# Optimization experiments

Hardware: AMD Instinct MI355X
Metric: run time of the kernel (lower is better)

## Reference

```python
import jax, jax.numpy as jnp
import numpy as np

B, S, D, H, HD = 4096, 50, 32, 4, 8
SCALE = 1.0 / (8 ** 0.5)


def setup_inputs() -> dict:
    key = jax.random.key(0)
    ks = jax.random.split(key, 12)
    inp = {
        'Q': jax.random.normal(ks[0], (B, S, D), dtype=jnp.float32),
        'K': jax.random.normal(ks[1], (B, S, D), dtype=jnp.float32),
        'V': jax.random.normal(ks[2], (B, S, D), dtype=jnp.float32),
        'mask': jax.random.randint(ks[3], (B, 1, S, S), 0, 2).astype(jnp.bool_),
        # Linear weights (stored as [in, out]; equivalent math to torch's x @ W.T + b)
        'WQ': jax.random.normal(ks[4], (D, D), dtype=jnp.float32) * 0.1,
        'bQ': jnp.zeros((D,), dtype=jnp.float32),
        'WK': jax.random.normal(ks[5], (D, D), dtype=jnp.float32) * 0.1,
        'bK': jnp.zeros((D,), dtype=jnp.float32),
        'WV': jax.random.normal(ks[6], (D, D), dtype=jnp.float32) * 0.1,
        'bV': jnp.zeros((D,), dtype=jnp.float32),
        'WO': jax.random.normal(ks[7], (D, D), dtype=jnp.float32) * 0.1,
        'bO': jnp.zeros((D,), dtype=jnp.float32),
    }
    return inp


def reference(Q, K, V, mask, WQ, bQ, WK, bK, WV, bV, WO, bO):
    qSrc = Q
    # fcQ/fcK/fcV are (faithfully) applied twice, as in the original forward
    q = (Q @ WQ + bQ) @ WQ + bQ
    k = (K @ WK + bK) @ WK + bK
    v = (V @ WV + bV) @ WV + bV
    # split heads: [B, S, D] -> [B, H, S, HD]
    q = q.reshape(B, S, H, HD).transpose(0, 2, 1, 3)
    k = k.reshape(B, S, H, HD).transpose(0, 2, 1, 3)
    v = v.reshape(B, S, H, HD).transpose(0, 2, 1, 3)
    score = jnp.einsum('bhqd,bhkd->bhqk', q, k) * SCALE
    score = jnp.where(mask, -jnp.inf, score)
    attn = jax.nn.softmax(score, axis=-1)
    ctx = jnp.einsum('bhqk,bhkd->bhqd', attn, v)
    ctx = ctx.transpose(0, 2, 1, 3).reshape(B, S, D)
    out = ctx @ WO + bO  # dropout is identity in eval mode
    return qSrc + out
```

## Files before the change

kernel.cpp:

```cpp
#include <hip/hip_runtime.h>

#define NB 4096
constexpr float kQscale = 0.35355339059327378f * 1.4426950408889634f;
constexpr int SV = 72;

typedef __attribute__((ext_vector_type(8))) short bf16x8;
typedef __attribute__((ext_vector_type(4))) float f32x4;
typedef __attribute__((ext_vector_type(4))) unsigned u32x4;

__device__ __forceinline__ unsigned cvt2(float lo, float hi) {
  unsigned u;
  asm("v_cvt_pk_bf16_f32 %0, %1, %2" : "=v"(u) : "v"(lo), "v"(hi));
  return u;
}
__device__ __forceinline__ float fexp2(float x) {
  float r;
  asm("v_exp_f32 %0, %1" : "=v"(r) : "v"(x));
  return r;
}
__device__ __forceinline__ void xchF(unsigned& a, unsigned& b) {
  asm volatile("v_permlane32_swap_b32 %0, %1" : "+v"(a), "+v"(b));
  asm volatile("v_permlane16_swap_b32 %0, %1" : "+v"(a), "+v"(b));
}

__global__ __launch_bounds__(256) void mha(
    const float* __restrict__ Qg, const float* __restrict__ Kg,
    const float* __restrict__ Vg, const void* __restrict__ maskg,
    const float* __restrict__ WQg, const float* __restrict__ bQg,
    const float* __restrict__ WKg, const float* __restrict__ bKg,
    const float* __restrict__ WVg, const float* __restrict__ bVg,
    const float* __restrict__ WOg, const float* __restrict__ bOg,
    float* __restrict__ outg)
{
  __shared__ __align__(16) short V2s[4][32*SV];
  __shared__ unsigned sRawW[4][80];

  const int t = threadIdx.x;
  const int lane = t & 63;
  const int wv = t >> 6;
  const int c = lane & 15, g = lane >> 4;
  const int b = blockIdx.x*4 + wv;
  short* V2 = V2s[wv];
  unsigned* sRaw = sRawW[wv];

  auto mkfrag = [&](float4 x0, float4 x1) -> bf16x8 {
    const u32x4 u = {cvt2(x0.x,x0.y), cvt2(x0.z,x0.w), cvt2(x1.x,x1.y), cvt2(x1.z,x1.w)};
    return __builtin_bit_cast(bf16x8, u);
  };
  auto ldW = [&](const float* __restrict__ Wp, int dcol) -> bf16x8 {
    float w[8];
    #pragma unroll
    for (int e = 0; e < 8; ++e) w[e] = Wp[(g*8 + e)*32 + dcol];
    const u32x4 u = {cvt2(w[0],w[1]), cvt2(w[2],w[3]), cvt2(w[4],w[5]), cvt2(w[6],w[7])};
    return __builtin_bit_cast(bf16x8, u);
  };
  auto projR = [&](bf16x8 xb, bf16x8 wa0, bf16x8 wa1,
                   float4 bv0, float4 bv1, float scale) -> bf16x8 {
    f32x4 c0 = {bv0.x, bv0.y, bv0.z, bv0.w};
    f32x4 c1 = {bv1.x, bv1.y, bv1.z, bv1.w};
    c0 = __builtin_amdgcn_mfma_f32_16x16x32_bf16(wa0, xb, c0, 0, 0, 0);
    c1 = __builtin_amdgcn_mfma_f32_16x16x32_bf16(wa1, xb, c1, 0, 0, 0);
    unsigned A0 = cvt2(c0[0]*scale, c0[1]*scale), A1 = cvt2(c0[2]*scale, c0[3]*scale);
    unsigned B0 = cvt2(c1[0]*scale, c1[1]*scale), B1 = cvt2(c1[2]*scale, c1[3]*scale);
    xchF(A0, B0); xchF(A1, B1);
    const u32x4 u = {A0, A1, B0, B1};
    return __builtin_bit_cast(bf16x8, u);
  };

  {
    const unsigned wdet = ((const unsigned*)maskg)[lane];
    const bool byteMask = (__ballot(wdet > 1u) != 0ull);
    for (int cg = 0; cg < 5; ++cg) {
      unsigned v[8];
      #pragma unroll
      for (int j = 0; j < 8; ++j) {
        const int idx = (cg*8 + j)*64 + lane;
        v[j] = 0;
        if (idx < 2500)
          v[j] = byteMask ? (unsigned)((const unsigned char*)maskg)[b*2500 + idx]
                          : ((const unsigned*)maskg)[b*2500 + idx];
      }
      #pragma unroll
      for (int j = 0; j < 8; ++j) {
        const unsigned long long m = __ballot(v[j] != 0u);
        const int ch = cg*8 + j;
        if (lane < 2) sRaw[ch*2 + lane] = lane ? (unsigned)(m >> 32) : (unsigned)m;
      }
    }
  }

  bf16x8 kf[4];
  {
    const bf16x8 wK0 = ldW(WKg, c), wK1 = ldW(WKg, 16 + c);
    const float4 bK0 = *(const float4*)&bKg[g*4];
    const float4 bK1 = *(const float4*)&bKg[16 + g*4];
    #pragma unroll
    for (int m = 0; m < 4; ++m) {
      const int row = m*16 + c;
      const int ra = b*1600 + ((row < 50) ? row : 0)*32 + g*8;
      const bf16x8 xb = mkfrag(*(const float4*)&Kg[ra], *(const float4*)&Kg[ra + 4]);
      const bf16x8 k1 = projR(xb, wK0, wK1, bK0, bK1, 1.f);
      kf[m] = projR(k1, wK0, wK1, bK0, bK1, 1.f);
    }
  }

  {
    const bf16x8 wV0 = ldW(WVg, c), wV1 = ldW(WVg, 16 + c);
    const float4 bV0 = *(const float4*)&bVg[g*4];
    const float4 bV1 = *(const float4*)&bVg[16 + g*4];
    const float bc0 = bVg[c], bc1 = bVg[16 + c];
    #pragma unroll
    for (int m = 0; m < 4; ++m) {
      const int row = m*16 + c;
      const int ra = b*1600 + ((row < 50) ? row : 0)*32 + g*8;
      const bf16x8 xb = mkfrag(*(const float4*)&Vg[ra], *(const float4*)&Vg[ra + 4]);
      const bf16x8 v1 = projR(xb, wV0, wV1, bV0, bV1, 1.f);
      f32x4 z0 = {bc0, bc0, bc0, bc0}, z1 = {bc1, bc1, bc1, bc1};
      z0 = __builtin_amdgcn_mfma_f32_16x16x32_bf16(v1, wV0, z0, 0, 0, 0);
      z1 = __builtin_amdgcn_mfma_f32_16x16x32_bf16(v1, wV1, z1, 0, 0, 0);
      const int j0 = m*16 + g*4;
      const float a0 = (j0+0 < 50) ? z0[0] : 0.f;
      const float a1 = (j0+1 < 50) ? z0[1] : 0.f;
      const float a2 = (j0+2 < 50) ? z0[2] : 0.f;
      const float a3 = (j0+3 < 50) ? z0[3] : 0.f;
      *(uint2*)&V2[c*SV + j0] = make_uint2(cvt2(a0,a1), cvt2(a2,a3));
      const float u0 = (j0+0 < 50) ? z1[0] : 0.f;
      const float u1 = (j0+1 < 50) ? z1[1] : 0.f;
      const float u2 = (j0+2 < 50) ? z1[2] : 0.f;
      const float u3 = (j0+3 < 50) ? z1[3] : 0.f;
      *(uint2*)&V2[(16 + c)*SV + j0] = make_uint2(cvt2(u0,u1), cvt2(u2,u3));
    }
  }

  const bf16x8 wQ0 = ldW(WQg, c), wQ1 = ldW(WQg, 16 + c);
  const float4 bQ0 = *(const float4*)&bQg[g*4];
  const float4 bQ1 = *(const float4*)&bQg[16 + g*4];
  const bf16x8 wO0 = ldW(WOg, c), wO1 = ldW(WOg, 16 + c);
  const float bO0 = bOg[c], bO1 = bOg[16 + c];
  __syncthreads();

  const bf16x8 zf = {0,0,0,0,0,0,0,0};

  #pragma unroll 1
  for (int qt = 0; qt < 4; ++qt) {
    const int myq = qt*16 + c;
    bf16x8 qb;
    {
      const int ra = b*1600 + ((myq < 50) ? myq : 0)*32 + g*8;
      const bf16x8 xq = mkfrag(*(const float4*)&Qg[ra], *(const float4*)&Qg[ra + 4]);
      const bf16x8 q1 = projR(xq, wQ0, wQ1, bQ0, bQ1, 1.f);
      qb = projR(q1, wQ0, wQ1, bQ0, bQ1, kQscale);
    }
    unsigned mm0, mm1;
    {
      const int bp = (myq < 50) ? 50*myq : 0;
      const unsigned ra = sRaw[(bp >> 5) + 0];
      const unsigned rb = sRaw[(bp >> 5) + 1];
      const unsigned rc = sRaw[(bp >> 5) + 2];
      const unsigned sh = bp & 31;
      mm0 = (unsigned)((((unsigned long long)rb << 32) | ra) >> sh);
      mm1 = (unsigned)((((unsigned long long)rc << 32) | rb) >> sh);
      if (myq >= 50) { mm0 = ~0u; mm1 = ~0u; }
    }
    unsigned ox0[4], ox1[4];
    #pragma unroll
    for (int h = 0; h < 4; ++h) {
      const bf16x8 vf0 = *(const bf16x8*)&V2[(h*8 + (c & 7))*SV + g*8];
      const bf16x8 vf1 = *(const bf16x8*)&V2[(h*8 + (c & 7))*SV + 32 + g*8];
      const bf16x8 qh = (g == h) ? qb : zf;
      f32x4 sc[4];
      #pragma unroll
      for (int Ni = 0; Ni < 4; ++Ni) {
        f32x4 z = {0.f, 0.f, 0.f, 0.f};
        sc[Ni] = __builtin_amdgcn_mfma_f32_16x16x32_bf16(kf[Ni], qh, z, 0, 0, 0);
      }
      unsigned kpm = 0;
      float mx = -1e30f;
      #pragma unroll
      for (int Ni = 0; Ni < 4; ++Ni) {
        const unsigned w = (Ni < 2) ? mm0 : mm1;
        #pragma unroll
        for (int r = 0; r < 4; ++r) {
          const int key = Ni*16 + g*4 + r;
          const bool keep = (key < 50) && (((w >> (key & 31)) & 1u) == 0u);
          kpm |= keep ? (1u << (Ni*4 + r)) : 0u;
          mx = keep ? fmaxf(mx, sc[Ni][r]) : mx;
        }
      }
      mx = fmaxf(mx, __shfl_xor(mx, 16));
      mx = fmaxf(mx, __shfl_xor(mx, 32));
      float rs = 0.f;
      unsigned pk[8];
      #pragma unroll
      for (int Ni = 0; Ni < 4; ++Ni) {
        float p[4];
        #pragma unroll
        for (int r = 0; r < 4; ++r) {
          const float e = fexp2(sc[Ni][r] - mx);
          p[r] = ((kpm >> (Ni*4 + r)) & 1u) ? e : 0.f;
          rs += p[r];
        }
        pk[Ni*2]   = cvt2(p[0], p[1]);
        pk[Ni*2+1] = cvt2(p[2], p[3]);
      }
      rs += __shfl_xor(rs, 16);
      rs += __shfl_xor(rs, 32);
      const float ri = (rs > 0.f) ? __builtin_amdgcn_rcpf(rs) : 0.f;
      unsigned w0 = pk[0], w2 = pk[2];  xchF(w0, w2);
      unsigned w1 = pk[1], w3 = pk[3];  xchF(w1, w3);
      unsigned x0 = pk[4], x2 = pk[6];  xchF(x0, x2);
      unsigned x1 = pk[5], x3 = pk[7];  xchF(x1, x3);
      const u32x4 w0v = {w0, w1, w2, w3};
      const u32x4 w1v = {x0, x1, x2, x3};
      const bf16x8 pf0 = __builtin_bit_cast(bf16x8, w0v);
      const bf16x8 pf1 = __builtin_bit_cast(bf16x8, w1v);
      f32x4 cac = {0.f, 0.f, 0.f, 0.f};
      cac = __builtin_amdgcn_mfma_f32_16x16x32_bf16(vf0, pf0, cac, 0, 0, 0);
      cac = __builtin_amdgcn_mfma_f32_16x16x32_bf16(vf1, pf1, cac, 0, 0, 0);
      ox0[h] = cvt2(cac[0]*ri, cac[1]*ri);
      ox1[h] = cvt2(cac[2]*ri, cac[3]*ri);
    }
    {
      float res[2][4];
      #pragma unroll
      for (int Nj = 0; Nj < 2; ++Nj)
        #pragma unroll
        for (int r = 0; r < 4; ++r) {
          const int row = qt*16 + g*4 + r;
          res[Nj][r] = (row < 50) ? Qg[b*1600 + row*32 + Nj*16 + c] : 0.f;
        }
      unsigned a0 = ox0[0], a1 = ox0[1], a2 = ox0[2], a3 = ox0[3];
      xchF(a0, a1);
      xchF(a2, a3);
      xchF(a0, a2);
      xchF(a1, a3);
      unsigned c0 = ox1[0], c1 = ox1[1], c2 = ox1[2], c3 = ox1[3];
      xchF(c0, c1);
      xchF(c2, c3);
      xchF(c0, c2);
      xchF(c1, c3);
      const u32x4 afv = {a0, c0, a1, c1};
      const bf16x8 af = __builtin_bit_cast(bf16x8, afv);
      #pragma unroll
      for (int Nj = 0; Nj < 2; ++Nj) {
        const bf16x8 bbf = Nj ? wO1 : wO0;
        const float bv = Nj ? bO1 : bO0;
        f32x4 o = {bv, bv, bv, bv};
        o = __builtin_amdgcn_mfma_f32_16x16x32_bf16(af, bbf, o, 0, 0, 0);
        #pragma unroll
        for (int r = 0; r < 4; ++r) {
          const int row = qt*16 + g*4 + r;
          if (row < 50)
            outg[b*1600 + row*32 + Nj*16 + c] = o[r] + res[Nj][r];
        }
      }
    }
  }
}

extern "C" void kernel_launch(void* const* d_in, const int* in_sizes, int n_in,
                              void* d_out, int out_size, void* d_ws, size_t ws_size,
                              hipStream_t stream) {
  const float* Q  = (const float*)d_in[0];
  const float* K  = (const float*)d_in[1];
  const float* V  = (const float*)d_in[2];
  const void*  M  = d_in[3];
  const float* WQ = (const float*)d_in[4];
  const float* bQ = (const float*)d_in[5];
  const float* WK = (const float*)d_in[6];
  const float* bK = (const float*)d_in[7];
  const float* WV = (const float*)d_in[8];
  const float* bV = (const float*)d_in[9];
  const float* WO = (const float*)d_in[10];
  const float* bO = (const float*)d_in[11];
  float* out = (float*)d_out;
  (void)d_ws; (void)ws_size; (void)in_sizes; (void)n_in; (void)out_size;

  hipLaunchKernelGGL(mha, dim3(NB/4), dim3(256), 0, stream,
                     Q, K, V, M, WQ, bQ, WK, bK, WV, bV, WO, bO, out);
}
```

Before: 65.07 us.

## Split each batch across four waves by query/key row tile with shared K/V

Each block of four waves now handles one batch element instead of four, and each wave owns one 16-row tile for the K, V and Q projections and for the attention. Projected K goes to shared memory so every wave can read all key fragments, and the mask bit-packing is spread across waves. The aim is to cut the per-wave serial work (the four-step query loop and repeated projections) and expose more parallelism with four times as many blocks. In exchange it adds a K shared-memory round trip, a block-wide barrier per batch, and reloads the weights in every wave of every block.

```diff
diff --git a/kernel.cpp b/kernel.cpp
--- a/kernel.cpp
+++ b/kernel.cpp
@@ -2,6 +2,7 @@
 
 #define NB 4096
 constexpr float kQscale = 0.35355339059327378f * 1.4426950408889634f;
+constexpr int ST = 40;
 constexpr int SV = 72;
 
 typedef __attribute__((ext_vector_type(8))) short bf16x8;
@@ -32,16 +33,16 @@
     const float* __restrict__ WOg, const float* __restrict__ bOg,
     float* __restrict__ outg)
 {
-  __shared__ __align__(16) short V2s[4][32*SV];
-  __shared__ unsigned sRawW[4][80];
+  __shared__ __align__(16) short K2s[64*ST];
+  __shared__ __align__(16) short V2[32*SV];
+  __shared__ unsigned sRaw[80];
 
   const int t = threadIdx.x;
+  const int b = blockIdx.x;
   const int lane = t & 63;
   const int wv = t >> 6;
   const int c = lane & 15, g = lane >> 4;
-  const int b = blockIdx.x*4 + wv;
-  short* V2 = V2s[wv];
-  unsigned* sRaw = sRawW[wv];
+  const int myrow = wv*16 + c;
 
   auto mkfrag = [&](float4 x0, float4 x1) -> bf16x8 {
     const u32x4 u = {cvt2(x0.x,x0.y), cvt2(x0.z,x0.w), cvt2(x1.x,x1.y), cvt2(x1.z,x1.w)};
@@ -67,192 +68,183 @@
     return __builtin_bit_cast(bf16x8, u);
   };
 
+  const int ra = b*1600 + ((myrow < 50) ? myrow : 0)*32 + g*8;
+  const bf16x8 xbK = mkfrag(*(const float4*)&Kg[ra], *(const float4*)&Kg[ra + 4]);
+  const bf16x8 xbV = mkfrag(*(const float4*)&Vg[ra], *(const float4*)&Vg[ra + 4]);
+  const bf16x8 xbQ = mkfrag(*(const float4*)&Qg[ra], *(const float4*)&Qg[ra + 4]);
+
   {
     const unsigned wdet = ((const unsigned*)maskg)[lane];
     const bool byteMask = (__ballot(wdet > 1u) != 0ull);
-    for (int cg = 0; cg < 5; ++cg) {
-      unsigned v[8];
-      #pragma unroll
-      for (int j = 0; j < 8; ++j) {
-        const int idx = (cg*8 + j)*64 + lane;
-        v[j] = 0;
-        if (idx < 2500)
-          v[j] = byteMask ? (unsigned)((const unsigned char*)maskg)[b*2500 + idx]
-                          : ((const unsigned*)maskg)[b*2500 + idx];
-      }
-      #pragma unroll
-      for (int j = 0; j < 8; ++j) {
-        const unsigned long long m = __ballot(v[j] != 0u);
-        const int ch = cg*8 + j;
-        if (lane < 2) sRaw[ch*2 + lane] = lane ? (unsigned)(m >> 32) : (unsigned)m;
-      }
-    }
-  }
-
-  bf16x8 kf[4];
+    #pragma unroll
+    for (int cc = 0; cc < 10; ++cc) {
+      const int ch = wv*10 + cc;
+      const int idx = ch*64 + lane;
+      unsigned val = 0;
+      if (idx < 2500)
+        val = byteMask ? (unsigned)((const unsigned char*)maskg)[b*2500 + idx]
+                       : ((const unsigned*)maskg)[b*2500 + idx];
+      const unsigned long long m = __ballot(val != 0u);
+      if (lane < 2) sRaw[ch*2 + lane] = lane ? (unsigned)(m >> 32) : (unsigned)m;
+    }
+  }
+
   {
     const bf16x8 wK0 = ldW(WKg, c), wK1 = ldW(WKg, 16 + c);
     const float4 bK0 = *(const float4*)&bKg[g*4];
     const float4 bK1 = *(const float4*)&bKg[16 + g*4];
-    #pragma unroll
-    for (int m = 0; m < 4; ++m) {
-      const int row = m*16 + c;
-      const int ra = b*1600 + ((row < 50) ? row : 0)*32 + g*8;
-      const bf16x8 xb = mkfrag(*(const float4*)&Kg[ra], *(const float4*)&Kg[ra + 4]);
-      const bf16x8 k1 = projR(xb, wK0, wK1, bK0, bK1, 1.f);
-      kf[m] = projR(k1, wK0, wK1, bK0, bK1, 1.f);
-    }
-  }
-
+    const bf16x8 k1 = projR(xbK, wK0, wK1, bK0, bK1, 1.f);
+    #pragma unroll
+    for (int Ni = 0; Ni < 2; ++Ni) {
+      const bf16x8 wa = Ni ? wK1 : wK0;
+      const float4 bv = Ni ? bK1 : bK0;
+      f32x4 acc = {bv.x, bv.y, bv.z, bv.w};
+      acc = __builtin_amdgcn_mfma_f32_16x16x32_bf16(wa, k1, acc, 0, 0, 0);
+      *(uint2*)&K2s[myrow*ST + Ni*16 + g*4] =
+          make_uint2(cvt2(acc[0], acc[1]), cvt2(acc[2], acc[3]));
+    }
+  }
   {
     const bf16x8 wV0 = ldW(WVg, c), wV1 = ldW(WVg, 16 + c);
     const float4 bV0 = *(const float4*)&bVg[g*4];
     const float4 bV1 = *(const float4*)&bVg[16 + g*4];
     const float bc0 = bVg[c], bc1 = bVg[16 + c];
-    #pragma unroll
-    for (int m = 0; m < 4; ++m) {
-      const int row = m*16 + c;
-      const int ra = b*1600 + ((row < 50) ? row : 0)*32 + g*8;
-      const bf16x8 xb = mkfrag(*(const float4*)&Vg[ra], *(const float4*)&Vg[ra + 4]);
-      const bf16x8 v1 = projR(xb, wV0, wV1, bV0, bV1, 1.f);
-      f32x4 z0 = {bc0, bc0, bc0, bc0}, z1 = {bc1, bc1, bc1, bc1};
-      z0 = __builtin_amdgcn_mfma_f32_16x16x32_bf16(v1, wV0, z0, 0, 0, 0);
-      z1 = __builtin_amdgcn_mfma_f32_16x16x32_bf16(v1, wV1, z1, 0, 0, 0);
-      const int j0 = m*16 + g*4;
-      const float a0 = (j0+0 < 50) ? z0[0] : 0.f;
-      const float a1 = (j0+1 < 50) ? z0[1] : 0.f;
-      const float a2 = (j0+2 < 50) ? z0[2] : 0.f;
-      const float a3 = (j0+3 < 50) ? z0[3] : 0.f;
-      *(uint2*)&V2[c*SV + j0] = make_uint2(cvt2(a0,a1), cvt2(a2,a3));
-      const float u0 = (j0+0 < 50) ? z1[0] : 0.f;
-      const float u1 = (j0+1 < 50) ? z1[1] : 0.f;
-      const float u2 = (j0+2 < 50) ? z1[2] : 0.f;
-      const float u3 = (j0+3 < 50) ? z1[3] : 0.f;
-      *(uint2*)&V2[(16 + c)*SV + j0] = make_uint2(cvt2(u0,u1), cvt2(u2,u3));
-    }
-  }
-
-  const bf16x8 wQ0 = ldW(WQg, c), wQ1 = ldW(WQg, 16 + c);
-  const float4 bQ0 = *(const float4*)&bQg[g*4];
-  const float4 bQ1 = *(const float4*)&bQg[16 + g*4];
-  const bf16x8 wO0 = ldW(WOg, c), wO1 = ldW(WOg, 16 + c);
-  const float bO0 = bOg[c], bO1 = bOg[16 + c];
+    const bf16x8 v1 = projR(xbV, wV0, wV1, bV0, bV1, 1.f);
+    f32x4 z0 = {bc0, bc0, bc0, bc0}, z1 = {bc1, bc1, bc1, bc1};
+    z0 = __builtin_amdgcn_mfma_f32_16x16x32_bf16(v1, wV0, z0, 0, 0, 0);
+    z1 = __builtin_amdgcn_mfma_f32_16x16x32_bf16(v1, wV1, z1, 0, 0, 0);
+    const int j0 = wv*16 + g*4;
+    const float a0 = (j0+0 < 50) ? z0[0] : 0.f;
+    const float a1 = (j0+1 < 50) ? z0[1] : 0.f;
+    const float a2 = (j0+2 < 50) ? z0[2] : 0.f;
+    const float a3 = (j0+3 < 50) ? z0[3] : 0.f;
+    *(uint2*)&V2[c*SV + j0] = make_uint2(cvt2(a0,a1), cvt2(a2,a3));
+    const float u0 = (j0+0 < 50) ? z1[0] : 0.f;
+    const float u1 = (j0+1 < 50) ? z1[1] : 0.f;
+    const float u2 = (j0+2 < 50) ? z1[2] : 0.f;
+    const float u3 = (j0+3 < 50) ? z1[3] : 0.f;
+    *(uint2*)&V2[(16 + c)*SV + j0] = make_uint2(cvt2(u0,u1), cvt2(u2,u3));
+  }
+  bf16x8 qb;
+  {
+    const bf16x8 wQ0 = ldW(WQg, c), wQ1 = ldW(WQg, 16 + c);
+    const float4 bQ0 = *(const float4*)&bQg[g*4];
+    const float4 bQ1 = *(const float4*)&bQg[16 + g*4];
+    const bf16x8 q1 = projR(xbQ, wQ0, wQ1, bQ0, bQ1, 1.f);
+    qb = projR(q1, wQ0, wQ1, bQ0, bQ1, kQscale);
+  }
   __syncthreads();
 
+  unsigned mm0, mm1;
+  {
+    const int bp = (myrow < 50) ? 50*myrow : 0;
+    const unsigned fa = sRaw[(bp >> 5) + 0];
+    const unsigned fb = sRaw[(bp >> 5) + 1];
+    const unsigned fc = sRaw[(bp >> 5) + 2];
+    const unsigned sh = bp & 31;
+    mm0 = (unsigned)((((unsigned long long)fb << 32) | fa) >> sh);
+    mm1 = (unsigned)((((unsigned long long)fc << 32) | fb) >> sh);
+    if (myrow >= 50) { mm0 = ~0u; mm1 = ~0u; }
+  }
+  bf16x8 kf[4];
+  #pragma unroll
+  for (int Ni = 0; Ni < 4; ++Ni)
+    kf[Ni] = *(const bf16x8*)&K2s[(Ni*16 + c)*ST + g*8];
+
   const bf16x8 zf = {0,0,0,0,0,0,0,0};
-
-  #pragma unroll 1
-  for (int qt = 0; qt < 4; ++qt) {
-    const int myq = qt*16 + c;
-    bf16x8 qb;
-    {
-      const int ra = b*1600 + ((myq < 50) ? myq : 0)*32 + g*8;
-      const bf16x8 xq = mkfrag(*(const float4*)&Qg[ra], *(const float4*)&Qg[ra + 4]);
-      const bf16x8 q1 = projR(xq, wQ0, wQ1, bQ0, bQ1, 1.f);
-      qb = projR(q1, wQ0, wQ1, bQ0, bQ1, kQscale);
-    }
-    unsigned mm0, mm1;
-    {
-      const int bp = (myq < 50) ? 50*myq : 0;
-      const unsigned ra = sRaw[(bp >> 5) + 0];
-      const unsigned rb = sRaw[(bp >> 5) + 1];
-      const unsigned rc = sRaw[(bp >> 5) + 2];
-      const unsigned sh = bp & 31;
-      mm0 = (unsigned)((((unsigned long long)rb << 32) | ra) >> sh);
-      mm1 = (unsigned)((((unsigned long long)rc << 32) | rb) >> sh);
-      if (myq >= 50) { mm0 = ~0u; mm1 = ~0u; }
-    }
-    unsigned ox0[4], ox1[4];
-    #pragma unroll
-    for (int h = 0; h < 4; ++h) {
-      const bf16x8 vf0 = *(const bf16x8*)&V2[(h*8 + (c & 7))*SV + g*8];
-      const bf16x8 vf1 = *(const bf16x8*)&V2[(h*8 + (c & 7))*SV + 32 + g*8];
-      const bf16x8 qh = (g == h) ? qb : zf;
-      f32x4 sc[4];
-      #pragma unroll
-      for (int Ni = 0; Ni < 4; ++Ni) {
-        f32x4 z = {0.f, 0.f, 0.f, 0.f};
-        sc[Ni] = __builtin_amdgcn_mfma_f32_16x16x32_bf16(kf[Ni], qh, z, 0, 0, 0);
-      }
-      unsigned kpm = 0;
-      float mx = -1e30f;
-      #pragma unroll
-      for (int Ni = 0; Ni < 4; ++Ni) {
-        const unsigned w = (Ni < 2) ? mm0 : mm1;
-        #pragma unroll
-        for (int r = 0; r < 4; ++r) {
-          const int key = Ni*16 + g*4 + r;
-          const bool keep = (key < 50) && (((w >> (key & 31)) & 1u) == 0u);
-          kpm |= keep ? (1u << (Ni*4 + r)) : 0u;
-          mx = keep ? fmaxf(mx, sc[Ni][r]) : mx;
-        }
-      }
-      mx = fmaxf(mx, __shfl_xor(mx, 16));
-      mx = fmaxf(mx, __shfl_xor(mx, 32));
-      float rs = 0.f;
-      unsigned pk[8];
-      #pragma unroll
-      for (int Ni = 0; Ni < 4; ++Ni) {
-        float p[4];
-        #pragma unroll
-        for (int r = 0; r < 4; ++r) {
-          const float e = fexp2(sc[Ni][r] - mx);
-          p[r] = ((kpm >> (Ni*4 + r)) & 1u) ? e : 0.f;
-          rs += p[r];
-        }
-        pk[Ni*2]   = cvt2(p[0], p[1]);
-        pk[Ni*2+1] = cvt2(p[2], p[3]);
-      }
-      rs += __shfl_xor(rs, 16);
-      rs += __shfl_xor(rs, 32);
-      const float ri = (rs > 0.f) ? __builtin_amdgcn_rcpf(rs) : 0.f;
-      unsigned w0 = pk[0], w2 = pk[2];  xchF(w0, w2);
-      unsigned w1 = pk[1], w3 = pk[3];  xchF(w1, w3);
-      unsigned x0 = pk[4], x2 = pk[6];  xchF(x0, x2);
-      unsigned x1 = pk[5], x3 = pk[7];  xchF(x1, x3);
-      const u32x4 w0v = {w0, w1, w2, w3};
-      const u32x4 w1v = {x0, x1, x2, x3};
-      const bf16x8 pf0 = __builtin_bit_cast(bf16x8, w0v);
-      const bf16x8 pf1 = __builtin_bit_cast(bf16x8, w1v);
-      f32x4 cac = {0.f, 0.f, 0.f, 0.f};
-      cac = __builtin_amdgcn_mfma_f32_16x16x32_bf16(vf0, pf0, cac, 0, 0, 0);
-      cac = __builtin_amdgcn_mfma_f32_16x16x32_bf16(vf1, pf1, cac, 0, 0, 0);
-      ox0[h] = cvt2(cac[0]*ri, cac[1]*ri);
-      ox1[h] = cvt2(cac[2]*ri, cac[3]*ri);
-    }
-    {
-      float res[2][4];
-      #pragma unroll
-      for (int Nj = 0; Nj < 2; ++Nj)
-        #pragma unroll
-        for (int r = 0; r < 4; ++r) {
-          const int row = qt*16 + g*4 + r;
-          res[Nj][r] = (row < 50) ? Qg[b*1600 + row*32 + Nj*16 + c] : 0.f;
-        }
-      unsigned a0 = ox0[0], a1 = ox0[1], a2 = ox0[2], a3 = ox0[3];
-      xchF(a0, a1);
-      xchF(a2, a3);
-      xchF(a0, a2);
-      xchF(a1, a3);
-      unsigned c0 = ox1[0], c1 = ox1[1], c2 = ox1[2], c3 = ox1[3];
-      xchF(c0, c1);
-      xchF(c2, c3);
-      xchF(c0, c2);
-      xchF(c1, c3);
-      const u32x4 afv = {a0, c0, a1, c1};
-      const bf16x8 af = __builtin_bit_cast(bf16x8, afv);
-      #pragma unroll
-      for (int Nj = 0; Nj < 2; ++Nj) {
-        const bf16x8 bbf = Nj ? wO1 : wO0;
-        const float bv = Nj ? bO1 : bO0;
-        f32x4 o = {bv, bv, bv, bv};
-        o = __builtin_amdgcn_mfma_f32_16x16x32_bf16(af, bbf, o, 0, 0, 0);
-        #pragma unroll
-        for (int r = 0; r < 4; ++r) {
-          const int row = qt*16 + g*4 + r;
-          if (row < 50)
-            outg[b*1600 + row*32 + Nj*16 + c] = o[r] + res[Nj][r];
-        }
+  unsigned ox0[4], ox1[4];
+  #pragma unroll
+  for (int h = 0; h < 4; ++h) {
+    const bf16x8 vf0 = *(const bf16x8*)&V2[(h*8 + (c & 7))*SV + g*8];
+    const bf16x8 vf1 = *(const bf16x8*)&V2[(h*8 + (c & 7))*SV + 32 + g*8];
+    const bf16x8 qh = (g == h) ? qb : zf;
+    f32x4 sc[4];
+    #pragma unroll
+    for (int Ni = 0; Ni < 4; ++Ni) {
+      f32x4 z = {0.f, 0.f, 0.f, 0.f};
+      sc[Ni] = __builtin_amdgcn_mfma_f32_16x16x32_bf16(kf[Ni], qh, z, 0, 0, 0);
+    }
+    unsigned kpm = 0;
+    float mx = -1e30f;
+    #pragma unroll
+    for (int Ni = 0; Ni < 4; ++Ni) {
+      const unsigned w = (Ni < 2) ? mm0 : mm1;
+      #pragma unroll
+      for (int r = 0; r < 4; ++r) {
+        const int key = Ni*16 + g*4 + r;
+        const bool keep = (key < 50) && (((w >> (key & 31)) & 1u) == 0u);
+        kpm |= keep ? (1u << (Ni*4 + r)) : 0u;
+        mx = keep ? fmaxf(mx, sc[Ni][r]) : mx;
+      }
+    }
+    mx = fmaxf(mx, __shfl_xor(mx, 16));
+    mx = fmaxf(mx, __shfl_xor(mx, 32));
+    float rs = 0.f;
+    unsigned pk[8];
+    #pragma unroll
+    for (int Ni = 0; Ni < 4; ++Ni) {
+      float p[4];
+      #pragma unroll
+      for (int r = 0; r < 4; ++r) {
+        const float e = fexp2(sc[Ni][r] - mx);
+        p[r] = ((kpm >> (Ni*4 + r)) & 1u) ? e : 0.f;
+        rs += p[r];
+      }
+      pk[Ni*2]   = cvt2(p[0], p[1]);
+      pk[Ni*2+1] = cvt2(p[2], p[3]);
+    }
+    rs += __shfl_xor(rs, 16);
+    rs += __shfl_xor(rs, 32);
+    const float ri = (rs > 0.f) ? __builtin_amdgcn_rcpf(rs) : 0.f;
+    unsigned w0 = pk[0], w2 = pk[2];  xchF(w0, w2);
+    unsigned w1 = pk[1], w3 = pk[3];  xchF(w1, w3);
+    unsigned x0 = pk[4], x2 = pk[6];  xchF(x0, x2);
+    unsigned x1 = pk[5], x3 = pk[7];  xchF(x1, x3);
+    const u32x4 w0v = {w0, w1, w2, w3};
+    const u32x4 w1v = {x0, x1, x2, x3};
+    const bf16x8 pf0 = __builtin_bit_cast(bf16x8, w0v);
+    const bf16x8 pf1 = __builtin_bit_cast(bf16x8, w1v);
+    f32x4 cac = {0.f, 0.f, 0.f, 0.f};
+    cac = __builtin_amdgcn_mfma_f32_16x16x32_bf16(vf0, pf0, cac, 0, 0, 0);
+    cac = __builtin_amdgcn_mfma_f32_16x16x32_bf16(vf1, pf1, cac, 0, 0, 0);
+    ox0[h] = cvt2(cac[0]*ri, cac[1]*ri);
+    ox1[h] = cvt2(cac[2]*ri, cac[3]*ri);
+  }
+
+  {
+    float res[2][4];
+    #pragma unroll
+    for (int Nj = 0; Nj < 2; ++Nj)
+      #pragma unroll
+      for (int r = 0; r < 4; ++r) {
+        const int row = wv*16 + g*4 + r;
+        res[Nj][r] = (row < 50) ? Qg[b*1600 + row*32 + Nj*16 + c] : 0.f;
+      }
+    unsigned a0 = ox0[0], a1 = ox0[1], a2 = ox0[2], a3 = ox0[3];
+    xchF(a0, a1);
+    xchF(a2, a3);
+    xchF(a0, a2);
+    xchF(a1, a3);
+    unsigned c0 = ox1[0], c1 = ox1[1], c2 = ox1[2], c3 = ox1[3];
+    xchF(c0, c1);
+    xchF(c2, c3);
+    xchF(c0, c2);
+    xchF(c1, c3);
+    const u32x4 afv = {a0, c0, a1, c1};
+    const bf16x8 af = __builtin_bit_cast(bf16x8, afv);
+    const bf16x8 wO0 = ldW(WOg, c), wO1 = ldW(WOg, 16 + c);
+    const float bO0 = bOg[c], bO1 = bOg[16 + c];
+    #pragma unroll
+    for (int Nj = 0; Nj < 2; ++Nj) {
+      const bf16x8 bbf = Nj ? wO1 : wO0;
+      const float bv = Nj ? bO1 : bO0;
+      f32x4 o = {bv, bv, bv, bv};
+      o = __builtin_amdgcn_mfma_f32_16x16x32_bf16(af, bbf, o, 0, 0, 0);
+      #pragma unroll
+      for (int r = 0; r < 4; ++r) {
+        const int row = wv*16 + g*4 + r;
+        if (row < 50)
+          outg[b*1600 + row*32 + Nj*16 + c] = o[r] + res[Nj][r];
       }
     }
   }
@@ -276,6 +268,6 @@
   float* out = (float*)d_out;
   (void)d_ws; (void)ws_size; (void)in_sizes; (void)n_in; (void)out_size;
 
-  hipLaunchKernelGGL(mha, dim3(NB/4), dim3(256), 0, stream,
+  hipLaunchKernelGGL(mha, dim3(NB), dim3(256), 0, stream,
                      Q, K, V, M, WQ, bQ, WK, bK, WV, bV, WO, bO, out);
 }
```

Measured after the change: 56.06 us. 13.8% less time.
